# Optimization experiments

Measured on AMD Instinct MI355X. Metric: run time of the kernel, lower is better.

## Reference

```python
import jax, jax.numpy as jnp
import numpy as np

N_NODES = 50000
N_EDGES = 3200000
N_GRAPHS = 50
IN_FEATS, HIDDEN, OUT_FEATS = 5, 64, 2


def setup_inputs() -> dict:
    key = jax.random.key(0)
    ks = jax.random.split(key, 10)
    x = jax.random.normal(ks[0], (N_NODES, IN_FEATS), dtype=jnp.float32)
    edge_index = jax.random.randint(ks[1], (2, N_EDGES), 0, N_NODES, dtype=jnp.int64)
    edge_attr = jax.random.uniform(ks[2], (N_EDGES, 1), dtype=jnp.float32)
    batch = jnp.sort(jax.random.randint(ks[3], (N_NODES,), 0, N_GRAPHS, dtype=jnp.int64))
    s1 = 1.0 / np.sqrt(IN_FEATS)
    s2 = 1.0 / np.sqrt(HIDDEN)
    W1 = jax.random.uniform(ks[4], (IN_FEATS, HIDDEN), jnp.float32, -s1, s1)
    b1 = jnp.zeros((HIDDEN,), jnp.float32)
    W2 = jax.random.uniform(ks[5], (HIDDEN, HIDDEN), jnp.float32, -s2, s2)
    b2 = jnp.zeros((HIDDEN,), jnp.float32)
    Wo = jax.random.uniform(ks[6], (HIDDEN, OUT_FEATS), jnp.float32, -s2, s2)
    bo = jax.random.uniform(ks[7], (OUT_FEATS,), jnp.float32, -s2, s2)
    return {"x": x, "edge_index": edge_index, "edge_attr": edge_attr, "batch": batch,
            "W1": W1, "b1": b1, "W2": W2, "b2": b2, "Wo": Wo, "bo": bo}


def _gcn_conv(x, src, dst, ew, W, b):
    # symmetric normalization: D^{-1/2} (A + I) D^{-1/2}, weighted degrees
    deg = jax.ops.segment_sum(ew, dst, num_segments=N_NODES)
    dinv = jnp.where(deg > 0, jax.lax.rsqrt(jnp.where(deg > 0, deg, 1.0)), 0.0)
    norm = dinv[src] * ew * dinv[dst]  # [E+N]
    h = x @ W                           # transform before propagate (PyG order)
    msg = h[src] * norm[:, None]        # gather + scale per edge
    out = jax.ops.segment_sum(msg, dst, num_segments=N_NODES)
    return out + b


def reference(x, edge_index, edge_attr, batch, W1, b1, W2, b2, Wo, bo):
    ew = edge_attr.squeeze(-1)
    loop = jnp.arange(N_NODES, dtype=edge_index.dtype)  # add self-loops (GCNConv default)
    src = jnp.concatenate([edge_index[0], loop])
    dst = jnp.concatenate([edge_index[1], loop])
    ew = jnp.concatenate([ew, jnp.ones((N_NODES,), ew.dtype)])
    h = jax.nn.relu(_gcn_conv(x, src, dst, ew, W1, b1))
    h = jax.nn.relu(_gcn_conv(h, src, dst, ew, W2, b2))
    # global mean pool over graphs
    sums = jax.ops.segment_sum(h, batch, num_segments=N_GRAPHS)
    cnt = jax.ops.segment_sum(jnp.ones((N_NODES,), h.dtype), batch, num_segments=N_GRAPHS)
    pooled = sums / jnp.maximum(cnt, 1.0)[:, None]
    return pooled @ Wo + bo  # [N_GRAPHS, OUT_FEATS]
```

## Files before the change

kernel.cpp:

```cpp
#include <hip/hip_runtime.h>
#include <hip/hip_fp16.h>

#define N_NODES 50000
#define N_EDGES 3200000
#define N_GRAPHS 50
#define IN_F 5
#define HID 64
#define OUT_F 2

#define BKT_SHIFT 5
#define BKT_W 32
#define NBKT 1563
#define NB1 250
#define EPB 12800
#define CAP 2560
#define TILE_SHIFT 12
#define NBIN (BKT_W * 16)
#define NWAVE 8192

__global__ void k_bhist(const int* dst, unsigned short* cw) {
    __shared__ int hist[NBKT];
    int t = threadIdx.x, blk = blockIdx.x;
    for (int b = t; b < NBKT; b += 1024) hist[b] = 0;
    __syncthreads();
    int base = blk * EPB;
    for (int k = t; k < EPB; k += 1024)
        atomicAdd(&hist[dst[base + k] >> BKT_SHIFT], 1);
    __syncthreads();
    for (int b = t; b < NBKT; b += 1024)
        cw[b * NB1 + blk] = (unsigned short)hist[b];
}

__global__ void k_bscanA(unsigned short* cw, int* total) {
    __shared__ int s[256];
    int t = threadIdx.x, b = blockIdx.x;
    int v = (t < NB1) ? (int)cw[b * NB1 + t] : 0;
    s[t] = v;
    __syncthreads();
    for (int off = 1; off < 256; off <<= 1) {
        int a = (t >= off) ? s[t - off] : 0;
        __syncthreads();
        s[t] += a;
        __syncthreads();
    }
    if (t < NB1) cw[b * NB1 + t] = (unsigned short)(s[t] - v);
    if (t == 255) total[b] = s[255];
}

__global__ void k_bscanB(const int* total, int* rpB) {
    __shared__ int s[256];
    int t = threadIdx.x;
    int v[7], sum = 0;
#pragma unroll
    for (int j = 0; j < 7; ++j) {
        int idx = t * 7 + j;
        v[j] = (idx < NBKT) ? total[idx] : 0;
        sum += v[j];
    }
    s[t] = sum;
    __syncthreads();
    for (int off = 1; off < 256; off <<= 1) {
        int a = (t >= off) ? s[t - off] : 0;
        __syncthreads();
        s[t] += a;
        __syncthreads();
    }
    int run = s[t] - sum;
#pragma unroll
    for (int j = 0; j < 7; ++j) {
        int idx = t * 7 + j;
        if (idx < NBKT) rpB[idx] = run;
        run += v[j];
    }
    if (t == 0) rpB[NBKT] = N_EDGES;
}

__global__ void k_bucket(const int* src, const int* dst, const float* ew,
                         const unsigned short* cw, const int* rpB, int2* bkt) {
    __shared__ int base[NBKT];
    __shared__ int off[NBKT];
    int t = threadIdx.x, blk = blockIdx.x;
    for (int b = t; b < NBKT; b += 1024) {
        base[b] = (int)cw[b * NB1 + blk] + rpB[b];
        off[b] = 0;
    }
    __syncthreads();
    int ebase = blk * EPB;
    for (int k = t; k < EPB; k += 1024) {
        int idx = ebase + k;
        int d = dst[idx];
        int b = d >> BKT_SHIFT;
        int sl = base[b] + atomicAdd(&off[b], 1);
        bkt[sl] = make_int2(src[idx] | ((d & (BKT_W - 1)) << 16), __float_as_int(ew[idx]));
    }
}

__global__ void k_bsort(const int* rpB, int2* bkt, int* rp2, int* rp2e, float* dinv) {
    __shared__ int2 ebuf[CAP];
    __shared__ int hist[NBIN];
    __shared__ int binoff[NBIN];
    __shared__ int s[256];
    __shared__ float wd[BKT_W];
    int t = threadIdx.x, b = blockIdx.x;
    int e0 = rpB[b], cnt = rpB[b + 1] - e0;
    for (int i = t; i < NBIN; i += 256) hist[i] = 0;
    if (t < BKT_W) wd[t] = 0.f;
    __syncthreads();
    for (int k = t; k < cnt; k += 256) {
        int2 e = bkt[e0 + k];
        ebuf[k] = e;
        int dl = (e.x >> 16) & (BKT_W - 1);
        int bin = (dl << 4) | ((e.x & 0xFFFF) >> TILE_SHIFT);
        atomicAdd(&hist[bin], 1);
        atomicAdd(&wd[dl], __int_as_float(e.y));
    }
    __syncthreads();
    int h0 = hist[2 * t], h1 = hist[2 * t + 1];
    int pv = h0 + h1;
    s[t] = pv;
    __syncthreads();
    for (int off = 1; off < 256; off <<= 1) {
        int a = (t >= off) ? s[t - off] : 0;
        __syncthreads();
        s[t] += a;
        __syncthreads();
    }
    int pe = s[t] - pv;
    binoff[2 * t] = pe;
    binoff[2 * t + 1] = pe + h0;
    __syncthreads();
    if (t < BKT_W) {
        int node = (b << BKT_SHIFT) + t;
        if (node < N_NODES) {
            int startl = binoff[t << 4];
            int endl = (t == BKT_W - 1) ? cnt : binoff[(t + 1) << 4];
            rp2[node]  = 2 * e0 + startl;
            rp2e[node] = 2 * e0 + endl;
            dinv[node] = rsqrtf(1.0f + wd[t]);
        }
    }
    __syncthreads();
    for (int k = t; k < cnt; k += 256) {
        int2 e = ebuf[k];
        int dl = (e.x >> 16) & (BKT_W - 1);
        int bin = (dl << 4) | ((e.x & 0xFFFF) >> TILE_SHIFT);
        int pos = atomicAdd(&binoff[bin], 1);
        unsigned short wh = __half_as_ushort(__float2half(__int_as_float(e.y)));
        ((int*)bkt)[2 * e0 + pos] = (e.x & 0xFFFF) | ((int)wh << 16);
    }
}

__global__ void k_xprep(const float* x, const float* dinv, __half* xp) {
    int i = blockIdx.x * 256 + threadIdx.x;
    if (i < N_NODES) {
        float di = dinv[i];
        const float* xi = &x[i * IN_F];
        __half* o = &xp[i * 8];
#pragma unroll
        for (int f = 0; f < IN_F; ++f) o[f] = __float2half(xi[f] * di);
        o[5] = o[6] = o[7] = __float2half(0.f);
    }
}

__global__ void k_p(const int* rp2, const int* rp2e, const int* pk,
                    const __half* xp, const float* dinv, float* p) {
    int node = blockIdx.x * 4 + (threadIdx.x >> 6);
    int lane = threadIdx.x & 63;
    if (node >= N_NODES) return;
    int b = rp2[node], en = rp2e[node];
    float a0 = 0.f, a1 = 0.f, a2 = 0.f, a3 = 0.f, a4 = 0.f;
    for (int k = b + lane; k < en; k += 64) {
        int e = pk[k];
        float w = __half2float(__ushort_as_half((unsigned short)((unsigned)e >> 16)));
        const __half* xs = &xp[(e & 0xFFFF) * 8];
        int4 xv = *reinterpret_cast<const int4*>(xs);
        __half2 p01 = *(__half2*)&xv.x;
        __half2 p23 = *(__half2*)&xv.y;
        __half2 p45 = *(__half2*)&xv.z;
        a0 += w * __half2float(p01.x); a1 += w * __half2float(p01.y);
        a2 += w * __half2float(p23.x); a3 += w * __half2float(p23.y);
        a4 += w * __half2float(p45.x);
    }
    for (int off = 32; off; off >>= 1) {
        a0 += __shfl_down(a0, off); a1 += __shfl_down(a1, off); a2 += __shfl_down(a2, off);
        a3 += __shfl_down(a3, off); a4 += __shfl_down(a4, off);
    }
    if (lane == 0) {
        float di = dinv[node];
        const __half* xn = &xp[node * 8];
        float* pp = &p[node * IN_F];
        pp[0] = di * (a0 + __half2float(xn[0]));
        pp[1] = di * (a1 + __half2float(xn[1]));
        pp[2] = di * (a2 + __half2float(xn[2]));
        pp[3] = di * (a3 + __half2float(xn[3]));
        pp[4] = di * (a4 + __half2float(xn[4]));
    }
}

__global__ void k_h1g(const float* p, const float* W1, const float* b1,
                      const float* W2, const float* dinv,
                      signed char* g8, float* rs) {
    __shared__ float W1s[IN_F * HID];
    __shared__ float W2s[HID * HID];
    __shared__ float b1s[HID];
    int t = threadIdx.x;
    for (int k = t; k < IN_F * HID; k += 256) W1s[k] = W1[k];
    for (int k = t; k < HID * HID; k += 256) W2s[k] = W2[k];
    if (t < HID) b1s[t] = b1[t];
    __syncthreads();
    int lane = t & 63;
    int wid = blockIdx.x * 4 + (t >> 6);
    int nw = gridDim.x * 4;
    for (int node = wid; node < N_NODES; node += nw) {
        const float* pp = &p[node * IN_F];
        float pv0 = pp[0], pv1 = pp[1], pv2 = pp[2], pv3 = pp[3], pv4 = pp[4];
        float h = b1s[lane] + pv0 * W1s[lane] + pv1 * W1s[64 + lane] + pv2 * W1s[128 + lane]
                + pv3 * W1s[192 + lane] + pv4 * W1s[256 + lane];
        h = fmaxf(h, 0.f);
        float acc = 0.f;
#pragma unroll
        for (int f = 0; f < HID; ++f) {
            float hf = __int_as_float(__builtin_amdgcn_readlane(__float_as_int(h), f));
            acc += hf * W2s[f * HID + lane];
        }
        float gv = acc * dinv[node];
        float am = fabsf(gv);
        for (int off = 32; off; off >>= 1) am = fmaxf(am, __shfl_xor(am, off));
        float inv = (am > 0.f) ? 127.0f / am : 0.f;
        g8[node * HID + lane] = (signed char)__float2int_rn(gv * inv);
        if (lane == 0) rs[node] = (am > 0.f) ? am * (1.0f / 127.0f) : 0.f;
    }
}

__global__ __launch_bounds__(256, 8) void k_h2g(const int* rp2, const int* rp2e,
                      const int* pk, const float* dinv, const signed char* g8,
                      const float* rs, const float* b2, const int* batch, float* pool) {
    int t = threadIdx.x, lane = t & 63;
    int wid = blockIdx.x * 4 + (t >> 6);
    int n0 = (int)(((long long)wid * N_NODES) / NWAVE);
    int n1 = (int)(((long long)(wid + 1) * N_NODES) / NWAVE);
    if (n0 >= n1) return;
    float bj = b2[lane];
    float accp = 0.f;
    int cur = batch[n0];
    for (int node = n0; node < n1; ++node) {
        int k0 = rp2[node], e1 = rp2e[node];
        float acc = (float)g8[node * HID + lane] * rs[node];
        for (; k0 < e1; k0 += 64) {
            int kk = k0 + lane;
            int ev = (kk < e1) ? pk[kk] : 0;
            int m = e1 - k0; if (m > 64) m = 64;
            int ng = (m + 15) >> 4;
            for (int q = 0; q < ng; ++q) {
                float vv[16], ww[16];
#pragma unroll
                for (int j = 0; j < 16; ++j) {
                    int u = __builtin_amdgcn_readlane(ev, q * 16 + j);
                    int sx = u & 0xFFFF;
                    float w = __half2float(__ushort_as_half((unsigned short)((unsigned)u >> 16)));
                    ww[j] = w * rs[sx];
                    vv[j] = (float)g8[sx * HID + lane];
                }
#pragma unroll
                for (int j = 0; j < 16; ++j) acc += vv[j] * ww[j];
            }
        }
        float h2 = fmaxf(dinv[node] * acc + bj, 0.f);
        int bb = batch[node];
        if (bb != cur) {
            atomicAdd(&pool[cur * HID + lane], accp);
            cur = bb;
            accp = 0.f;
        }
        accp += h2;
    }
    atomicAdd(&pool[cur * HID + lane], accp);
}

__device__ int lowb(const int* a, int n, int v) {
    int lo = 0, hi = n;
    while (lo < hi) { int m = (lo + hi) >> 1; if (a[m] < v) lo = m + 1; else hi = m; }
    return lo;
}

__global__ void k_out(const float* pool, const int* batch, const float* Wo,
                      const float* bo, float* out) {
    int t = blockIdx.x * blockDim.x + threadIdx.x;
    if (t < N_GRAPHS * OUT_F) {
        int gi = t / OUT_F, k = t % OUT_F;
        int c = lowb(batch, N_NODES, gi + 1) - lowb(batch, N_NODES, gi);
        float cf = fmaxf((float)c, 1.0f);
        float acc = bo[k];
        for (int f = 0; f < HID; ++f)
            acc += (pool[gi * HID + f] / cf) * Wo[f * OUT_F + k];
        out[t] = acc;
    }
}

extern "C" void kernel_launch(void* const* d_in, const int* in_sizes, int n_in,
                              void* d_out, int out_size, void* d_ws, size_t ws_size,
                              hipStream_t stream) {
    const float* x   = (const float*)d_in[0];
    const int*   ei  = (const int*)d_in[1];
    const float* ea  = (const float*)d_in[2];
    const int*   bat = (const int*)d_in[3];
    const float* W1  = (const float*)d_in[4];
    const float* b1  = (const float*)d_in[5];
    const float* W2  = (const float*)d_in[6];
    const float* b2  = (const float*)d_in[7];
    const float* Wo  = (const float*)d_in[8];
    const float* bo  = (const float*)d_in[9];
    float* out = (float*)d_out;

    const int* src = ei;
    const int* dst = ei + N_EDGES;

    float* ws = (float*)d_ws;
    int*   rpB   = (int*)ws;
    int*   rp2   = (int*)(ws + 1568);
    int*   rp2e  = (int*)(ws + 51584);
    float* dinv  = ws + 101600;
    float* rs    = ws + 151616;
    float* pool  = ws + 201632;
    int*   total = (int*)(ws + 201632);
    unsigned short* cw = (unsigned short*)(ws + 204832);
    float* p     = ws + 204832;
    int2*  bkt   = (int2*)(ws + 454832);
    signed char* g8 = (signed char*)(ws + 6854832);
    __half* xp   = (__half*)(ws + 7654832);

    k_bhist <<<NB1, 1024, 0, stream>>>(dst, cw);
    k_bscanA<<<NBKT, 256, 0, stream>>>(cw, total);
    k_bscanB<<<1, 256, 0, stream>>>(total, rpB);
    hipMemsetAsync(pool, 0, N_GRAPHS * HID * sizeof(float), stream);
    k_bucket<<<NB1, 1024, 0, stream>>>(src, dst, ea, cw, rpB, bkt);
    k_bsort <<<NBKT, 256, 0, stream>>>(rpB, bkt, rp2, rp2e, dinv);
    k_xprep <<<(N_NODES + 255) / 256, 256, 0, stream>>>(x, dinv, xp);
    k_p     <<<(N_NODES + 3) / 4, 256, 0, stream>>>(rp2, rp2e, (const int*)bkt, xp, dinv, p);
    k_h1g   <<<1024, 256, 0, stream>>>(p, W1, b1, W2, dinv, g8, rs);
    k_h2g   <<<NWAVE / 4, 256, 0, stream>>>(rp2, rp2e, (const int*)bkt, dinv, g8, rs, b2, bat, pool);
    k_out   <<<1, 128, 0, stream>>>(pool, bat, Wo, bo, out);
}
```

Baseline: 307.0 us.

## Pack edges into 32-bit words and gather 4 features per lane in layer-2

The bucket stage now quantizes edge weights to 11 bits and packs them with source and local destination into a single 32-bit word, halving bucket traffic and ebuf shared memory. Degree sums become integer atomics. Layer-2 aggregation switches to offset-binary uint8 features, with each lane loading 4 features of one of 4 edges at a time via a dword gather. It corrects the offset with a weight sum and reduces across lane groups with shuffles. This cuts gather instruction count per edge but adds weight-quantization error and a cross-group reduction per node.

```diff
diff --git a/kernel.cpp b/kernel.cpp
--- a/kernel.cpp
+++ b/kernel.cpp
@@ -76,7 +76,7 @@
 }
 
 __global__ void k_bucket(const int* src, const int* dst, const float* ew,
-                         const unsigned short* cw, const int* rpB, int2* bkt) {
+                         const unsigned short* cw, const int* rpB, int* bkt) {
     __shared__ int base[NBKT];
     __shared__ int off[NBKT];
     int t = threadIdx.x, blk = blockIdx.x;
@@ -91,28 +91,29 @@
         int d = dst[idx];
         int b = d >> BKT_SHIFT;
         int sl = base[b] + atomicAdd(&off[b], 1);
-        bkt[sl] = make_int2(src[idx] | ((d & (BKT_W - 1)) << 16), __float_as_int(ew[idx]));
-    }
-}
-
-__global__ void k_bsort(const int* rpB, int2* bkt, int* rp2, int* rp2e, float* dinv) {
-    __shared__ int2 ebuf[CAP];
+        int wq = (int)rintf(ew[idx] * 2047.0f);
+        bkt[sl] = src[idx] | ((d & (BKT_W - 1)) << 16) | (wq << 21);
+    }
+}
+
+__global__ void k_bsort(const int* rpB, int* bkt, int* rp2, int* rp2e, float* dinv) {
+    __shared__ int ebuf[CAP];
     __shared__ int hist[NBIN];
     __shared__ int binoff[NBIN];
     __shared__ int s[256];
-    __shared__ float wd[BKT_W];
+    __shared__ int wdI[BKT_W];
     int t = threadIdx.x, b = blockIdx.x;
     int e0 = rpB[b], cnt = rpB[b + 1] - e0;
     for (int i = t; i < NBIN; i += 256) hist[i] = 0;
-    if (t < BKT_W) wd[t] = 0.f;
+    if (t < BKT_W) wdI[t] = 0;
     __syncthreads();
     for (int k = t; k < cnt; k += 256) {
-        int2 e = bkt[e0 + k];
-        ebuf[k] = e;
-        int dl = (e.x >> 16) & (BKT_W - 1);
-        int bin = (dl << 4) | ((e.x & 0xFFFF) >> TILE_SHIFT);
+        int u = bkt[e0 + k];
+        ebuf[k] = u;
+        int dl = (u >> 16) & (BKT_W - 1);
+        int bin = (dl << 4) | ((u & 0xFFFF) >> TILE_SHIFT);
         atomicAdd(&hist[bin], 1);
-        atomicAdd(&wd[dl], __int_as_float(e.y));
+        atomicAdd(&wdI[dl], (int)((unsigned)u >> 21));
     }
     __syncthreads();
     int h0 = hist[2 * t], h1 = hist[2 * t + 1];
@@ -134,19 +135,20 @@
         if (node < N_NODES) {
             int startl = binoff[t << 4];
             int endl = (t == BKT_W - 1) ? cnt : binoff[(t + 1) << 4];
-            rp2[node]  = 2 * e0 + startl;
-            rp2e[node] = 2 * e0 + endl;
-            dinv[node] = rsqrtf(1.0f + wd[t]);
+            rp2[node]  = e0 + startl;
+            rp2e[node] = e0 + endl;
+            dinv[node] = rsqrtf(1.0f + (float)wdI[t] * (1.0f / 2047.0f));
         }
     }
     __syncthreads();
     for (int k = t; k < cnt; k += 256) {
-        int2 e = ebuf[k];
-        int dl = (e.x >> 16) & (BKT_W - 1);
-        int bin = (dl << 4) | ((e.x & 0xFFFF) >> TILE_SHIFT);
+        int u = ebuf[k];
+        int dl = (u >> 16) & (BKT_W - 1);
+        int bin = (dl << 4) | ((u & 0xFFFF) >> TILE_SHIFT);
         int pos = atomicAdd(&binoff[bin], 1);
-        unsigned short wh = __half_as_ushort(__float2half(__int_as_float(e.y)));
-        ((int*)bkt)[2 * e0 + pos] = (e.x & 0xFFFF) | ((int)wh << 16);
+        float wf = (float)((unsigned)u >> 21) * (1.0f / 2047.0f);
+        unsigned short wh = __half_as_ushort(__float2half(wf));
+        bkt[e0 + pos] = (u & 0xFFFF) | ((int)wh << 16);
     }
 }
 
@@ -199,7 +201,7 @@
 
 __global__ void k_h1g(const float* p, const float* W1, const float* b1,
                       const float* W2, const float* dinv,
-                      signed char* g8, float* rs) {
+                      unsigned char* g8u, float* rs) {
     __shared__ float W1s[IN_F * HID];
     __shared__ float W2s[HID * HID];
     __shared__ float b1s[HID];
@@ -227,54 +229,86 @@
         float am = fabsf(gv);
         for (int off = 32; off; off >>= 1) am = fmaxf(am, __shfl_xor(am, off));
         float inv = (am > 0.f) ? 127.0f / am : 0.f;
-        g8[node * HID + lane] = (signed char)__float2int_rn(gv * inv);
+        g8u[node * HID + lane] = (unsigned char)(__float2int_rn(gv * inv) + 128);
         if (lane == 0) rs[node] = (am > 0.f) ? am * (1.0f / 127.0f) : 0.f;
     }
 }
 
+#define EDGE4_BODY(UU)                                                         \
+    {                                                                          \
+        int u_ = (UU);                                                         \
+        float w_ = __half2float(__ushort_as_half((unsigned short)((unsigned)u_ >> 16))); \
+        float wwv_ = w_ * rs[u_ & 0xFFFF];                                     \
+        unsigned dw_ = *(const unsigned*)&g8u[(u_ & 0xFFFF) * HID + fo];       \
+        a0 += wwv_ * (float)(dw_ & 0xFF);                                      \
+        a1 += wwv_ * (float)((dw_ >> 8) & 0xFF);                               \
+        a2 += wwv_ * (float)((dw_ >> 16) & 0xFF);                              \
+        a3 += wwv_ * (float)(dw_ >> 24);                                       \
+        sww += wwv_;                                                           \
+    }
+
 __global__ __launch_bounds__(256, 8) void k_h2g(const int* rp2, const int* rp2e,
-                      const int* pk, const float* dinv, const signed char* g8,
+                      const int* pk, const float* dinv, const unsigned char* g8u,
                       const float* rs, const float* b2, const int* batch, float* pool) {
     int t = threadIdx.x, lane = t & 63;
+    int grp = lane >> 4;
+    int fo = (lane & 15) << 2;
     int wid = blockIdx.x * 4 + (t >> 6);
     int n0 = (int)(((long long)wid * N_NODES) / NWAVE);
     int n1 = (int)(((long long)(wid + 1) * N_NODES) / NWAVE);
     if (n0 >= n1) return;
-    float bj = b2[lane];
-    float accp = 0.f;
+    float4 bj = *reinterpret_cast<const float4*>(&b2[fo]);
+    float p0 = 0.f, p1 = 0.f, p2 = 0.f, p3 = 0.f;
     int cur = batch[n0];
     for (int node = n0; node < n1; ++node) {
-        int k0 = rp2[node], e1 = rp2e[node];
-        float acc = (float)g8[node * HID + lane] * rs[node];
-        for (; k0 < e1; k0 += 64) {
+        unsigned dws = *(const unsigned*)&g8u[node * HID + fo];
+        float wq4 = 0.25f * rs[node];
+        float a0 = wq4 * (float)(dws & 0xFF);
+        float a1 = wq4 * (float)((dws >> 8) & 0xFF);
+        float a2 = wq4 * (float)((dws >> 16) & 0xFF);
+        float a3 = wq4 * (float)(dws >> 24);
+        float sww = wq4;
+        for (int k0 = rp2[node], e1 = rp2e[node]; k0 < e1; k0 += 64) {
             int kk = k0 + lane;
             int ev = (kk < e1) ? pk[kk] : 0;
             int m = e1 - k0; if (m > 64) m = 64;
-            int ng = (m + 15) >> 4;
-            for (int q = 0; q < ng; ++q) {
-                float vv[16], ww[16];
-#pragma unroll
-                for (int j = 0; j < 16; ++j) {
-                    int u = __builtin_amdgcn_readlane(ev, q * 16 + j);
-                    int sx = u & 0xFFFF;
-                    float w = __half2float(__ushort_as_half((unsigned short)((unsigned)u >> 16)));
-                    ww[j] = w * rs[sx];
-                    vv[j] = (float)g8[sx * HID + lane];
-                }
-#pragma unroll
-                for (int j = 0; j < 16; ++j) acc += vv[j] * ww[j];
+            if (m == 64) {
+#pragma unroll
+                for (int q = 0; q < 16; ++q) EDGE4_BODY(__shfl(ev, (q << 2) | grp))
+            } else {
+                int ng = (m + 3) >> 2;
+                for (int q = 0; q < ng; ++q) EDGE4_BODY(__shfl(ev, (q << 2) | grp))
             }
         }
-        float h2 = fmaxf(dinv[node] * acc + bj, 0.f);
+#pragma unroll
+        for (int off = 16; off <= 32; off <<= 1) {
+            a0 += __shfl_xor(a0, off); a1 += __shfl_xor(a1, off);
+            a2 += __shfl_xor(a2, off); a3 += __shfl_xor(a3, off);
+            sww += __shfl_xor(sww, off);
+        }
+        float di = dinv[node];
+        float corr = 128.0f * sww;
+        float h0 = fmaxf(di * (a0 - corr) + bj.x, 0.f);
+        float h1 = fmaxf(di * (a1 - corr) + bj.y, 0.f);
+        float h2 = fmaxf(di * (a2 - corr) + bj.z, 0.f);
+        float h3 = fmaxf(di * (a3 - corr) + bj.w, 0.f);
         int bb = batch[node];
         if (bb != cur) {
-            atomicAdd(&pool[cur * HID + lane], accp);
+            if (lane < 16) {
+                float* pb = &pool[cur * HID + fo];
+                atomicAdd(pb + 0, p0); atomicAdd(pb + 1, p1);
+                atomicAdd(pb + 2, p2); atomicAdd(pb + 3, p3);
+            }
             cur = bb;
-            accp = 0.f;
-        }
-        accp += h2;
-    }
-    atomicAdd(&pool[cur * HID + lane], accp);
+            p0 = p1 = p2 = p3 = 0.f;
+        }
+        p0 += h0; p1 += h1; p2 += h2; p3 += h3;
+    }
+    if (lane < 16) {
+        float* pb = &pool[cur * HID + fo];
+        atomicAdd(pb + 0, p0); atomicAdd(pb + 1, p1);
+        atomicAdd(pb + 2, p2); atomicAdd(pb + 3, p3);
+    }
 }
 
 __device__ int lowb(const int* a, int n, int v) {
@@ -325,9 +359,9 @@
     int*   total = (int*)(ws + 201632);
     unsigned short* cw = (unsigned short*)(ws + 204832);
     float* p     = ws + 204832;
-    int2*  bkt   = (int2*)(ws + 454832);
-    signed char* g8 = (signed char*)(ws + 6854832);
-    __half* xp   = (__half*)(ws + 7654832);
+    int*   bkt   = (int*)(ws + 454832);
+    unsigned char* g8u = (unsigned char*)(ws + 3654832);
+    __half* xp   = (__half*)(ws + 4454832);
 
     k_bhist <<<NB1, 1024, 0, stream>>>(dst, cw);
     k_bscanA<<<NBKT, 256, 0, stream>>>(cw, total);
@@ -336,8 +370,8 @@
     k_bucket<<<NB1, 1024, 0, stream>>>(src, dst, ea, cw, rpB, bkt);
     k_bsort <<<NBKT, 256, 0, stream>>>(rpB, bkt, rp2, rp2e, dinv);
     k_xprep <<<(N_NODES + 255) / 256, 256, 0, stream>>>(x, dinv, xp);
-    k_p     <<<(N_NODES + 3) / 4, 256, 0, stream>>>(rp2, rp2e, (const int*)bkt, xp, dinv, p);
-    k_h1g   <<<1024, 256, 0, stream>>>(p, W1, b1, W2, dinv, g8, rs);
-    k_h2g   <<<NWAVE / 4, 256, 0, stream>>>(rp2, rp2e, (const int*)bkt, dinv, g8, rs, b2, bat, pool);
+    k_p     <<<(N_NODES + 3) / 4, 256, 0, stream>>>(rp2, rp2e, bkt, xp, dinv, p);
+    k_h1g   <<<1024, 256, 0, stream>>>(p, W1, b1, W2, dinv, g8u, rs);
+    k_h2g   <<<NWAVE / 4, 256, 0, stream>>>(rp2, rp2e, bkt, dinv, g8u, rs, b2, bat, pool);
     k_out   <<<1, 128, 0, stream>>>(pool, bat, Wo, bo, out);
 }
```

Result: faster. 279.8 us (-8.9%).
